# Kernel tuning notes

Hardware: AMD Instinct MI355X
Metric: run time of the kernel (lower is better)

The kernel has to match this reference:

```python
import jax, jax.numpy as jnp
import numpy as np

TAU = 1.5      # lif_tau
V_TH = 1.0     # spikingjelly default v_threshold
EPS = 1e-5     # BatchNorm eps
ALPHA = 4.0    # spikingjelly default sigmoid surrogate alpha

@jax.custom_vjp
def spike_fn(x):
    return (x >= 0.0).astype(x.dtype)

def _spike_fwd(x):
    return spike_fn(x), x

def _spike_bwd(x, g):
    s = jax.nn.sigmoid(ALPHA * x)
    return (g * ALPHA * s * (1.0 - s),)

spike_fn.defvjp(_spike_fwd, _spike_bwd)

def lif(x):
    # x: [T, B, C, N]; hard reset to 0, decay_input=True, detach_reset=True
    def step(v, xt):
        v = v + (xt - v) / TAU
        s = spike_fn(v - V_TH)
        sd = jax.lax.stop_gradient(s)
        v = (1.0 - sd) * v
        return v, s
    _, spikes = jax.lax.scan(step, jnp.zeros_like(x[0]), x)
    return spikes

def bn(x, gamma, beta, mean, var):
    # eval-mode BatchNorm1d over channel dim of [B, C, L]
    inv = gamma * jax.lax.rsqrt(var + EPS)
    return x * inv[None, :, None] + (beta - mean * inv)[None, :, None]

def setup_inputs() -> dict:
    key = jax.random.key(0)
    ks = jax.random.split(key, 13)
    B, C, T, N, H = 8, 256, 4, 4096, 1024
    return {
        "x": jax.random.normal(ks[0], (B, C, T, N), jnp.float32),
        "fc1_w": jax.random.normal(ks[1], (H, C), jnp.float32) * 0.05,
        "fc1_b": jax.random.normal(ks[2], (H,), jnp.float32) * 0.05,
        "fc2_w": jax.random.normal(ks[3], (C, H), jnp.float32) * 0.05,
        "fc2_b": jax.random.normal(ks[4], (C,), jnp.float32) * 0.05,
        "bn1_gamma": jax.random.uniform(ks[5], (H,), jnp.float32, 0.5, 1.5),
        "bn1_beta": jax.random.normal(ks[6], (H,), jnp.float32) * 0.1,
        "bn1_mean": jax.random.normal(ks[7], (H,), jnp.float32) * 0.1,
        "bn1_var": jax.random.uniform(ks[8], (H,), jnp.float32, 0.5, 1.5),
        "bn2_gamma": jax.random.uniform(ks[9], (C,), jnp.float32, 0.5, 1.5),
        "bn2_beta": jax.random.normal(ks[10], (C,), jnp.float32) * 0.1,
        "bn2_mean": jax.random.normal(ks[11], (C,), jnp.float32) * 0.1,
        "bn2_var": jax.random.uniform(ks[12], (C,), jnp.float32, 0.5, 1.5),
    }

def reference(x, fc1_w, fc1_b, fc2_w, fc2_b,
              bn1_gamma, bn1_beta, bn1_mean, bn1_var,
              bn2_gamma, bn2_beta, bn2_mean, bn2_var):
    B, C, T, N = x.shape
    H = fc1_w.shape[0]
    # fc2_bn on raw input, then LIF over T
    h = bn(x.reshape(B, C, T * N), bn2_gamma, bn2_beta, bn2_mean, bn2_var)
    h = h.reshape(B, C, T, N).transpose(2, 0, 1, 3)          # [T,B,C,N]
    h = lif(h).transpose(1, 2, 0, 3).reshape(B, C, T * N)    # [B,C,TN]
    # fc1: 1x1 conv == GEMM over channels
    h = jnp.einsum('hc,bcl->bhl', fc1_w, h) + fc1_b[None, :, None]
    h = bn(h, bn1_gamma, bn1_beta, bn1_mean, bn1_var)
    h = h.reshape(B, H, T, N).transpose(2, 0, 1, 3)          # [T,B,H,N]
    h = lif(h).transpose(1, 2, 0, 3).reshape(B, H, T * N)    # [B,H,TN]
    # fc2
    h = jnp.einsum('ch,bhl->bcl', fc2_w, h) + fc2_b[None, :, None]
    return h.reshape(B, C, T, N)
```

## Files before the change

kernel.cpp:

```cpp
#include <hip/hip_runtime.h>

#define BB 8
#define CC 256
#define TT 4
#define NNv 4096
#define HH 1024
#define LLv (TT*NNv)

typedef short bf16x8 __attribute__((ext_vector_type(8)));
typedef float f32x4 __attribute__((ext_vector_type(4)));

static __device__ __forceinline__ float bfbits2f(unsigned short h) {
    return __uint_as_float(((unsigned int)h) << 16);
}
static __device__ __forceinline__ unsigned short f2bf(float f) {
    unsigned int u = __float_as_uint(f);
    return (unsigned short)((u + 0x7FFFu + ((u >> 16) & 1u)) >> 16);
}
static __device__ __forceinline__ int permpos(int j) { return (j >> 1) + ((j & 1) << 2); }

static __device__ __forceinline__ uint4 spikes8_to_bf16(unsigned long long d) {
    unsigned int lo = (unsigned int)d, hi = (unsigned int)(d >> 32);
    uint4 o;
    o.x = (lo & 0x10001u) * 0x3F80u;
    o.y = (hi & 0x10001u) * 0x3F80u;
    o.z = ((lo >> 8) & 0x10001u) * 0x3F80u;
    o.w = ((hi >> 8) & 0x10001u) * 0x3F80u;
    return o;
}

__global__ __launch_bounds__(256) void k_prep1(const float* __restrict__ w,
                                               unsigned short* __restrict__ wf)
{
    int i = blockIdx.x * 256 + threadIdx.x;
    int h = i >> 8, c = i & 255;
    int ht = h >> 6, hr = h & 63, g = hr >> 4, ln = hr & 15;
    int ko = c >> 6, cr = c & 63, kb = cr >> 5, q = (cr >> 3) & 3, j = c & 7;
    size_t base = (((((size_t)ht * 4 + ko) * 2 + kb) * 4 + g) * 64 + q * 16 + ln) * 8 + permpos(j);
    const size_t WS = 262144;
    float x = w[i];
    unsigned short hi = f2bf(x); float r  = __fsub_rn(x, bfbits2f(hi));
    unsigned short md = f2bf(r); float r2 = __fsub_rn(r, bfbits2f(md));
    unsigned short lo = f2bf(r2);
    wf[base] = hi; wf[WS + base] = md; wf[2 * WS + base] = lo;
}

__global__ __launch_bounds__(256) void k_prep2(const float* __restrict__ w,
                                               unsigned short* __restrict__ wf)
{
    int i = blockIdx.x * 256 + threadIdx.x;
    int c = i >> 10, h = i & 1023;
    int ct = c >> 6, cr = c & 63, g = cr >> 4, ln = cr & 15;
    int ko = h >> 7, hr = h & 127, kb = hr >> 5, q = (hr >> 3) & 3, j = h & 7;
    size_t base = (((((size_t)ct * 8 + ko) * 4 + kb) * 4 + g) * 64 + q * 16 + ln) * 8 + permpos(j);
    const size_t WS = 262144;
    float x = w[i];
    unsigned short hi = f2bf(x); float r = __fsub_rn(x, bfbits2f(hi));
    unsigned short lo = f2bf(r);
    wf[base] = hi; wf[WS + base] = lo;
}

__global__ __launch_bounds__(256) void k_bn2_lif_t(
    const float* __restrict__ x,
    const float* __restrict__ g, const float* __restrict__ be,
    const float* __restrict__ mu, const float* __restrict__ va,
    unsigned char* __restrict__ s1T)
{
    __shared__ unsigned char ts[TT][64][80];
    int tx = threadIdx.x;
    int n0 = blockIdx.x * 64;
    int c0 = blockIdx.y * 64;
    int b  = blockIdx.z;
    int cl = tx >> 2, np = tx & 3;
    int c = c0 + cl;
    float rsq = __fdiv_rn(1.0f, __fsqrt_rn(__fadd_rn(va[c], 1e-5f)));
    float inv = __fmul_rn(g[c], rsq);
    float add = __fsub_rn(be[c], __fmul_rn(mu[c], inv));
    size_t xb = ((size_t)(b * CC + c) * TT) * NNv + n0 + np * 16;
    float v[16];
    #pragma unroll
    for (int i = 0; i < 16; i++) v[i] = 0.0f;
    #pragma unroll
    for (int t = 0; t < TT; t++) {
        float4 p[4];
        #pragma unroll
        for (int k = 0; k < 4; k++) p[k] = *(const float4*)(x + xb + (size_t)t * NNv + 4 * k);
        const float* xp = (const float*)p;
        unsigned int ob[4] = {0, 0, 0, 0};
        #pragma unroll
        for (int i = 0; i < 16; i++) {
            float y = __fadd_rn(__fmul_rn(xp[i], inv), add);
            float vv = __fadd_rn(v[i], __fdiv_rn(__fsub_rn(y, v[i]), 1.5f));
            bool sp = vv >= 1.0f;
            v[i] = sp ? 0.0f : vv;
            if (sp) ob[i >> 2] |= 1u << (8 * (i & 3));
        }
        uint4 pk; pk.x = ob[0]; pk.y = ob[1]; pk.z = ob[2]; pk.w = ob[3];
        *(uint4*)&ts[t][cl][np * 16] = pk;
    }
    __syncthreads();
    int nl = tx >> 2, cp = tx & 3;
    #pragma unroll
    for (int t = 0; t < TT; t++) {
        unsigned int u[4];
        #pragma unroll
        for (int kk = 0; kk < 4; kk++) {
            u[kk] = (unsigned int)ts[t][cp * 16 + kk * 4 + 0][nl]
                  | ((unsigned int)ts[t][cp * 16 + kk * 4 + 1][nl] << 8)
                  | ((unsigned int)ts[t][cp * 16 + kk * 4 + 2][nl] << 16)
                  | ((unsigned int)ts[t][cp * 16 + kk * 4 + 3][nl] << 24);
        }
        uint4 pk; pk.x = u[0]; pk.y = u[1]; pk.z = u[2]; pk.w = u[3];
        *(uint4*)(s1T + ((size_t)(b * TT + t) * NNv + n0 + nl) * CC + c0 + cp * 16) = pk;
    }
}

__global__ __launch_bounds__(256) void k_gemm1_lif(
    const unsigned short* __restrict__ w1f,
    const float* __restrict__ b1,
    const float* __restrict__ g1, const float* __restrict__ be1,
    const float* __restrict__ mu1, const float* __restrict__ va1,
    const unsigned char* __restrict__ s1T, unsigned char* __restrict__ s2T)
{
    __shared__ unsigned short Ss[TT][64][72];
    const int tx = threadIdx.x;
    const int n0 = blockIdx.x * 64;
    const int ht = blockIdx.y;
    const int b  = blockIdx.z;
    const int lane = tx & 63, w = tx >> 6;
    const int q = lane >> 4, ln = lane & 15;
    const int mh = (w & 1) * 32, wn = (w >> 1) * 32;
    const int h0 = ht * 64;
    const size_t WS = 262144;

    f32x4 acc[TT][2][2];
    #pragma unroll
    for (int t = 0; t < TT; t++)
    #pragma unroll
    for (int mi = 0; mi < 2; mi++)
    #pragma unroll
    for (int ni = 0; ni < 2; ni++)
        acc[t][mi][ni] = (f32x4){0.f, 0.f, 0.f, 0.f};

    for (int ko = 0; ko < 4; ko++) {
        __syncthreads();
        #pragma unroll
        for (int i = 0; i < 8; i++) {
            int task = i * 256 + tx;
            int cb = task & 7, nr = (task >> 3) & 63, t = task >> 9;
            unsigned long long d = *(const unsigned long long*)(
                s1T + ((size_t)(b * TT + t) * NNv + n0 + nr) * CC + ko * 64 + cb * 8);
            *(uint4*)&Ss[t][nr][cb * 8] = spikes8_to_bf16(d);
        }
        __syncthreads();
        #pragma unroll
        for (int kb = 0; kb < 2; kb++) {
            bf16x8 wf[2][3];
            #pragma unroll
            for (int mi = 0; mi < 2; mi++) {
                int gg = (mh >> 4) + mi;
                size_t fbase = (((((size_t)ht * 4 + ko) * 2 + kb) * 4 + gg) * 64 + lane) * 8;
                #pragma unroll
                for (int s = 0; s < 3; s++)
                    wf[mi][s] = *(const bf16x8*)(w1f + s * WS + fbase);
            }
            #pragma unroll
            for (int t = 0; t < TT; t++) {
                bf16x8 sf0 = *(const bf16x8*)&Ss[t][wn + ln][kb * 32 + q * 8];
                bf16x8 sf1 = *(const bf16x8*)&Ss[t][wn + 16 + ln][kb * 32 + q * 8];
                #pragma unroll
                for (int s = 0; s < 3; s++) {
                    acc[t][0][0] = __builtin_amdgcn_mfma_f32_16x16x32_bf16(wf[0][s], sf0, acc[t][0][0], 0, 0, 0);
                    acc[t][0][1] = __builtin_amdgcn_mfma_f32_16x16x32_bf16(wf[0][s], sf1, acc[t][0][1], 0, 0, 0);
                    acc[t][1][0] = __builtin_amdgcn_mfma_f32_16x16x32_bf16(wf[1][s], sf0, acc[t][1][0], 0, 0, 0);
                    acc[t][1][1] = __builtin_amdgcn_mfma_f32_16x16x32_bf16(wf[1][s], sf1, acc[t][1][1], 0, 0, 0);
                }
            }
        }
    }

    #pragma unroll
    for (int mi = 0; mi < 2; mi++) {
        float invr[4], addr_[4], biasr[4];
        #pragma unroll
        for (int r = 0; r < 4; r++) {
            int h = h0 + mh + mi * 16 + q * 4 + r;
            float rsq = __fdiv_rn(1.0f, __fsqrt_rn(__fadd_rn(va1[h], 1e-5f)));
            invr[r] = __fmul_rn(g1[h], rsq);
            addr_[r] = __fsub_rn(be1[h], __fmul_rn(mu1[h], invr[r]));
            biasr[r] = b1[h];
        }
        #pragma unroll
        for (int ni = 0; ni < 2; ni++) {
            int l_n = n0 + wn + ni * 16 + ln;
            float v4[4] = {0.f, 0.f, 0.f, 0.f};
            #pragma unroll
            for (int t = 0; t < TT; t++) {
                unsigned int pk = 0;
                #pragma unroll
                for (int r = 0; r < 4; r++) {
                    float h1 = __fadd_rn(acc[t][mi][ni][r], biasr[r]);
                    float y  = __fadd_rn(__fmul_rn(h1, invr[r]), addr_[r]);
                    float vv = __fadd_rn(v4[r], __fdiv_rn(__fsub_rn(y, v4[r]), 1.5f));
                    bool sp = vv >= 1.0f;
                    v4[r] = sp ? 0.0f : vv;
                    if (sp) pk |= (1u << (8 * r));
                }
                *(unsigned int*)(s2T + ((size_t)b * LLv + t * NNv + l_n) * HH
                                 + h0 + mh + mi * 16 + q * 4) = pk;
            }
        }
    }
}

__global__ __launch_bounds__(256) void k_gemm2(
    const unsigned short* __restrict__ w2f,
    const float* __restrict__ b2c,
    const unsigned char* __restrict__ s2T, float* __restrict__ outp)
{
    __shared__ unsigned short Ss[128][136];
    const int tx = threadIdx.x;
    const int l0 = blockIdx.x * 128;
    const int ct = blockIdx.y;
    const int b  = blockIdx.z;
    const int lane = tx & 63, w = tx >> 6;
    const int q = lane >> 4, ln = lane & 15;
    const int mc = (w & 1) * 32, wl = (w >> 1) * 64;
    const size_t WS = 262144;

    f32x4 acc[2][4];
    #pragma unroll
    for (int mi = 0; mi < 2; mi++)
    #pragma unroll
    for (int ni = 0; ni < 4; ni++)
        acc[mi][ni] = (f32x4){0.f, 0.f, 0.f, 0.f};

    for (int ko = 0; ko < 8; ko++) {
        __syncthreads();
        #pragma unroll
        for (int i = 0; i < 8; i++) {
            int task = i * 256 + tx;
            int hb = task & 15, lr = task >> 4;
            unsigned long long d = *(const unsigned long long*)(
                s2T + ((size_t)b * LLv + l0 + lr) * HH + ko * 128 + hb * 8);
            *(uint4*)&Ss[lr][hb * 8] = spikes8_to_bf16(d);
        }
        __syncthreads();
        #pragma unroll
        for (int kb = 0; kb < 4; kb++) {
            bf16x8 wf[2][2];
            #pragma unroll
            for (int mi = 0; mi < 2; mi++) {
                int gg = (mc >> 4) + mi;
                size_t fbase = (((((size_t)ct * 8 + ko) * 4 + kb) * 4 + gg) * 64 + lane) * 8;
                #pragma unroll
                for (int s = 0; s < 2; s++)
                    wf[mi][s] = *(const bf16x8*)(w2f + s * WS + fbase);
            }
            bf16x8 sf[4];
            #pragma unroll
            for (int ni = 0; ni < 4; ni++)
                sf[ni] = *(const bf16x8*)&Ss[wl + ni * 16 + ln][kb * 32 + q * 8];
            #pragma unroll
            for (int s = 0; s < 2; s++)
            #pragma unroll
            for (int mi = 0; mi < 2; mi++)
            #pragma unroll
            for (int ni = 0; ni < 4; ni++)
                acc[mi][ni] = __builtin_amdgcn_mfma_f32_16x16x32_bf16(wf[mi][s], sf[ni], acc[mi][ni], 0, 0, 0);
        }
    }
    #pragma unroll
    for (int mi = 0; mi < 2; mi++)
    #pragma unroll
    for (int r = 0; r < 4; r++) {
        int c = ct * 64 + mc + mi * 16 + q * 4 + r;
        float bias = b2c[c];
        #pragma unroll
        for (int ni = 0; ni < 4; ni++) {
            int l = l0 + wl + ni * 16 + ln;
            outp[((size_t)b * CC + c) * LLv + l] = __fadd_rn(acc[mi][ni][r], bias);
        }
    }
}

extern "C" void kernel_launch(void* const* d_in, const int* in_sizes, int n_in,
                              void* d_out, int out_size, void* d_ws, size_t ws_size,
                              hipStream_t stream) {
    const float* x    = (const float*)d_in[0];
    const float* fc1w = (const float*)d_in[1];
    const float* fc1b = (const float*)d_in[2];
    const float* fc2w = (const float*)d_in[3];
    const float* fc2b = (const float*)d_in[4];
    const float* g1   = (const float*)d_in[5];
    const float* be1  = (const float*)d_in[6];
    const float* mu1  = (const float*)d_in[7];
    const float* va1  = (const float*)d_in[8];
    const float* g2   = (const float*)d_in[9];
    const float* be2  = (const float*)d_in[10];
    const float* mu2  = (const float*)d_in[11];
    const float* va2  = (const float*)d_in[12];

    unsigned short* w1f = (unsigned short*)d_ws;
    unsigned short* w2f = w1f + (size_t)3 * 262144;
    unsigned char*  s1T = (unsigned char*)(w2f + (size_t)2 * 262144);
    unsigned char*  s2T = s1T + (size_t)BB * CC * LLv;
    float* outp = (float*)d_out;

    hipLaunchKernelGGL(k_prep1, dim3(1024), dim3(256), 0, stream, fc1w, w1f);
    hipLaunchKernelGGL(k_prep2, dim3(1024), dim3(256), 0, stream, fc2w, w2f);
    hipLaunchKernelGGL(k_bn2_lif_t, dim3(NNv / 64, CC / 64, BB), dim3(256), 0, stream,
                       x, g2, be2, mu2, va2, s1T);
    hipLaunchKernelGGL(k_gemm1_lif, dim3(NNv / 64, HH / 64, BB), dim3(256), 0, stream,
                       w1f, fc1b, g1, be1, mu1, va1, s1T, s2T);
    hipLaunchKernelGGL(k_gemm2, dim3(LLv / 128, CC / 64, BB), dim3(256), 0, stream,
                       w2f, fc2b, s2T, outp);
}
```

Baseline: 622.2 us.

## Store spikes as pre-permuted bf16 and load MFMA operands directly from global

Spike tensors are now written as bf16 values in the MFMA operand permutation, so the GEMM kernels read B fragments straight from global memory instead of staging and expanding them through LDS with barriers. The GEMMs are launched in chunks of two batches, and the grid is reordered so blocks sharing an activation tile run adjacently. This keeps the per-chunk s2 intermediate small enough to stay in cache. Launch bounds request higher occupancy. The cost is doubled spike storage and more launches.

```diff
diff --git a/kernel.cpp b/kernel.cpp
--- a/kernel.cpp
+++ b/kernel.cpp
@@ -19,16 +19,6 @@
 }
 static __device__ __forceinline__ int permpos(int j) { return (j >> 1) + ((j & 1) << 2); }
 
-static __device__ __forceinline__ uint4 spikes8_to_bf16(unsigned long long d) {
-    unsigned int lo = (unsigned int)d, hi = (unsigned int)(d >> 32);
-    uint4 o;
-    o.x = (lo & 0x10001u) * 0x3F80u;
-    o.y = (hi & 0x10001u) * 0x3F80u;
-    o.z = ((lo >> 8) & 0x10001u) * 0x3F80u;
-    o.w = ((hi >> 8) & 0x10001u) * 0x3F80u;
-    return o;
-}
-
 __global__ __launch_bounds__(256) void k_prep1(const float* __restrict__ w,
                                                unsigned short* __restrict__ wf)
 {
@@ -64,7 +54,7 @@
     const float* __restrict__ x,
     const float* __restrict__ g, const float* __restrict__ be,
     const float* __restrict__ mu, const float* __restrict__ va,
-    unsigned char* __restrict__ s1T)
+    unsigned short* __restrict__ s1b)
 {
     __shared__ unsigned char ts[TT][64][80];
     int tx = threadIdx.x;
@@ -100,33 +90,31 @@
     }
     __syncthreads();
     int nl = tx >> 2, cp = tx & 3;
+    const int perm8[8] = {0, 2, 4, 6, 1, 3, 5, 7};
     #pragma unroll
     for (int t = 0; t < TT; t++) {
-        unsigned int u[4];
-        #pragma unroll
-        for (int kk = 0; kk < 4; kk++) {
-            u[kk] = (unsigned int)ts[t][cp * 16 + kk * 4 + 0][nl]
-                  | ((unsigned int)ts[t][cp * 16 + kk * 4 + 1][nl] << 8)
-                  | ((unsigned int)ts[t][cp * 16 + kk * 4 + 2][nl] << 16)
-                  | ((unsigned int)ts[t][cp * 16 + kk * 4 + 3][nl] << 24);
-        }
-        uint4 pk; pk.x = u[0]; pk.y = u[1]; pk.z = u[2]; pk.w = u[3];
-        *(uint4*)(s1T + ((size_t)(b * TT + t) * NNv + n0 + nl) * CC + c0 + cp * 16) = pk;
-    }
-}
-
-__global__ __launch_bounds__(256) void k_gemm1_lif(
+        unsigned short sh[16];
+        #pragma unroll
+        for (int p = 0; p < 16; p++)
+            sh[p] = ts[t][cp * 16 + (p & 8) + perm8[p & 7]][nl] ? 0x3F80 : 0;
+        unsigned short* op = s1b + ((size_t)(b * TT + t) * NNv + n0 + nl) * CC + c0 + cp * 16;
+        *(uint4*)op = *(uint4*)&sh[0];
+        *(uint4*)(op + 8) = *(uint4*)&sh[8];
+    }
+}
+
+__global__ __launch_bounds__(256, 3) void k_gemm1_lif(
     const unsigned short* __restrict__ w1f,
     const float* __restrict__ b1,
     const float* __restrict__ g1, const float* __restrict__ be1,
     const float* __restrict__ mu1, const float* __restrict__ va1,
-    const unsigned char* __restrict__ s1T, unsigned char* __restrict__ s2T)
-{
-    __shared__ unsigned short Ss[TT][64][72];
+    const unsigned short* __restrict__ s1b, unsigned short* __restrict__ s2b, int boff)
+{
     const int tx = threadIdx.x;
-    const int n0 = blockIdx.x * 64;
-    const int ht = blockIdx.y;
-    const int b  = blockIdx.z;
+    const int ht = blockIdx.x;
+    const int n0 = blockIdx.y * 64;
+    const int bl = blockIdx.z;
+    const int b  = boff + bl;
     const int lane = tx & 63, w = tx >> 6;
     const int q = lane >> 4, ln = lane & 15;
     const int mh = (w & 1) * 32, wn = (w >> 1) * 32;
@@ -142,32 +130,25 @@
     for (int ni = 0; ni < 2; ni++)
         acc[t][mi][ni] = (f32x4){0.f, 0.f, 0.f, 0.f};
 
+    #pragma unroll
     for (int ko = 0; ko < 4; ko++) {
-        __syncthreads();
-        #pragma unroll
-        for (int i = 0; i < 8; i++) {
-            int task = i * 256 + tx;
-            int cb = task & 7, nr = (task >> 3) & 63, t = task >> 9;
-            unsigned long long d = *(const unsigned long long*)(
-                s1T + ((size_t)(b * TT + t) * NNv + n0 + nr) * CC + ko * 64 + cb * 8);
-            *(uint4*)&Ss[t][nr][cb * 8] = spikes8_to_bf16(d);
-        }
-        __syncthreads();
         #pragma unroll
         for (int kb = 0; kb < 2; kb++) {
             bf16x8 wf[2][3];
             #pragma unroll
             for (int mi = 0; mi < 2; mi++) {
                 int gg = (mh >> 4) + mi;
-                size_t fbase = (((((size_t)ht * 4 + ko) * 2 + kb) * 4 + gg) * 64 + lane) * 8;
+                size_t fb = (((((size_t)ht * 4 + ko) * 2 + kb) * 4 + gg) * 64 + lane) * 8;
                 #pragma unroll
                 for (int s = 0; s < 3; s++)
-                    wf[mi][s] = *(const bf16x8*)(w1f + s * WS + fbase);
+                    wf[mi][s] = *(const bf16x8*)(w1f + s * WS + fb);
             }
             #pragma unroll
             for (int t = 0; t < TT; t++) {
-                bf16x8 sf0 = *(const bf16x8*)&Ss[t][wn + ln][kb * 32 + q * 8];
-                bf16x8 sf1 = *(const bf16x8*)&Ss[t][wn + 16 + ln][kb * 32 + q * 8];
+                const unsigned short* bp = s1b
+                    + ((size_t)(b * TT + t) * NNv + n0 + wn) * CC + ko * 64 + kb * 32 + q * 8;
+                bf16x8 sf0 = *(const bf16x8*)(bp + ln * CC);
+                bf16x8 sf1 = *(const bf16x8*)(bp + (16 + ln) * CC);
                 #pragma unroll
                 for (int s = 0; s < 3; s++) {
                     acc[t][0][0] = __builtin_amdgcn_mfma_f32_16x16x32_bf16(wf[0][s], sf0, acc[t][0][0], 0, 0, 0);
@@ -190,13 +171,15 @@
             addr_[r] = __fsub_rn(be1[h], __fmul_rn(mu1[h], invr[r]));
             biasr[r] = b1[h];
         }
+        int hgrp = h0 + mh + mi * 16 + (q >> 1) * 8;
+        int hsub = (q & 1) * 2;
         #pragma unroll
         for (int ni = 0; ni < 2; ni++) {
             int l_n = n0 + wn + ni * 16 + ln;
             float v4[4] = {0.f, 0.f, 0.f, 0.f};
             #pragma unroll
             for (int t = 0; t < TT; t++) {
-                unsigned int pk = 0;
+                unsigned short sv[4];
                 #pragma unroll
                 for (int r = 0; r < 4; r++) {
                     float h1 = __fadd_rn(acc[t][mi][ni][r], biasr[r]);
@@ -204,25 +187,26 @@
                     float vv = __fadd_rn(v4[r], __fdiv_rn(__fsub_rn(y, v4[r]), 1.5f));
                     bool sp = vv >= 1.0f;
                     v4[r] = sp ? 0.0f : vv;
-                    if (sp) pk |= (1u << (8 * r));
+                    sv[r] = sp ? 0x3F80 : 0;
                 }
-                *(unsigned int*)(s2T + ((size_t)b * LLv + t * NNv + l_n) * HH
-                                 + h0 + mh + mi * 16 + q * 4) = pk;
-            }
-        }
-    }
-}
-
-__global__ __launch_bounds__(256) void k_gemm2(
+                unsigned short* op = s2b + ((size_t)bl * LLv + t * NNv + l_n) * HH + hgrp + hsub;
+                *(unsigned int*)op       = (unsigned int)sv[0] | ((unsigned int)sv[2] << 16);
+                *(unsigned int*)(op + 4) = (unsigned int)sv[1] | ((unsigned int)sv[3] << 16);
+            }
+        }
+    }
+}
+
+__global__ __launch_bounds__(256, 4) void k_gemm2(
     const unsigned short* __restrict__ w2f,
     const float* __restrict__ b2c,
-    const unsigned char* __restrict__ s2T, float* __restrict__ outp)
-{
-    __shared__ unsigned short Ss[128][136];
+    const unsigned short* __restrict__ s2b, float* __restrict__ outp, int boff)
+{
     const int tx = threadIdx.x;
-    const int l0 = blockIdx.x * 128;
-    const int ct = blockIdx.y;
-    const int b  = blockIdx.z;
+    const int ct = blockIdx.x;
+    const int l0 = blockIdx.y * 128;
+    const int bl = blockIdx.z;
+    const int b  = boff + bl;
     const int lane = tx & 63, w = tx >> 6;
     const int q = lane >> 4, ln = lane & 15;
     const int mc = (w & 1) * 32, wl = (w >> 1) * 64;
@@ -235,32 +219,25 @@
     for (int ni = 0; ni < 4; ni++)
         acc[mi][ni] = (f32x4){0.f, 0.f, 0.f, 0.f};
 
+    #pragma unroll
     for (int ko = 0; ko < 8; ko++) {
-        __syncthreads();
-        #pragma unroll
-        for (int i = 0; i < 8; i++) {
-            int task = i * 256 + tx;
-            int hb = task & 15, lr = task >> 4;
-            unsigned long long d = *(const unsigned long long*)(
-                s2T + ((size_t)b * LLv + l0 + lr) * HH + ko * 128 + hb * 8);
-            *(uint4*)&Ss[lr][hb * 8] = spikes8_to_bf16(d);
-        }
-        __syncthreads();
         #pragma unroll
         for (int kb = 0; kb < 4; kb++) {
             bf16x8 wf[2][2];
             #pragma unroll
             for (int mi = 0; mi < 2; mi++) {
                 int gg = (mc >> 4) + mi;
-                size_t fbase = (((((size_t)ct * 8 + ko) * 4 + kb) * 4 + gg) * 64 + lane) * 8;
+                size_t fb = (((((size_t)ct * 8 + ko) * 4 + kb) * 4 + gg) * 64 + lane) * 8;
                 #pragma unroll
                 for (int s = 0; s < 2; s++)
-                    wf[mi][s] = *(const bf16x8*)(w2f + s * WS + fbase);
+                    wf[mi][s] = *(const bf16x8*)(w2f + s * WS + fb);
             }
             bf16x8 sf[4];
+            const unsigned short* bp = s2b
+                + ((size_t)bl * LLv + l0 + wl) * HH + ko * 128 + kb * 32 + q * 8;
             #pragma unroll
             for (int ni = 0; ni < 4; ni++)
-                sf[ni] = *(const bf16x8*)&Ss[wl + ni * 16 + ln][kb * 32 + q * 8];
+                sf[ni] = *(const bf16x8*)(bp + (ni * 16 + ln) * HH);
             #pragma unroll
             for (int s = 0; s < 2; s++)
             #pragma unroll
@@ -301,18 +278,21 @@
     const float* mu2  = (const float*)d_in[11];
     const float* va2  = (const float*)d_in[12];
 
+    const size_t WS = 262144;
     unsigned short* w1f = (unsigned short*)d_ws;
-    unsigned short* w2f = w1f + (size_t)3 * 262144;
-    unsigned char*  s1T = (unsigned char*)(w2f + (size_t)2 * 262144);
-    unsigned char*  s2T = s1T + (size_t)BB * CC * LLv;
+    unsigned short* w2f = w1f + 3 * WS;
+    unsigned short* s1b = w2f + 2 * WS;
+    unsigned short* s2b = s1b + (size_t)BB * CC * LLv;
     float* outp = (float*)d_out;
 
     hipLaunchKernelGGL(k_prep1, dim3(1024), dim3(256), 0, stream, fc1w, w1f);
     hipLaunchKernelGGL(k_prep2, dim3(1024), dim3(256), 0, stream, fc2w, w2f);
     hipLaunchKernelGGL(k_bn2_lif_t, dim3(NNv / 64, CC / 64, BB), dim3(256), 0, stream,
-                       x, g2, be2, mu2, va2, s1T);
-    hipLaunchKernelGGL(k_gemm1_lif, dim3(NNv / 64, HH / 64, BB), dim3(256), 0, stream,
-                       w1f, fc1b, g1, be1, mu1, va1, s1T, s2T);
-    hipLaunchKernelGGL(k_gemm2, dim3(LLv / 128, CC / 64, BB), dim3(256), 0, stream,
-                       w2f, fc2b, s2T, outp);
-}
+                       x, g2, be2, mu2, va2, s1b);
+    for (int boff = 0; boff < BB; boff += 2) {
+        hipLaunchKernelGGL(k_gemm1_lif, dim3(HH / 64, NNv / 64, 2), dim3(256), 0, stream,
+                           w1f, fc1b, g1, be1, mu1, va1, s1b, s2b, boff);
+        hipLaunchKernelGGL(k_gemm2, dim3(CC / 64, LLv / 128, 2), dim3(256), 0, stream,
+                           w2f, fc2b, s2b, outp, boff);
+    }
+}
```

After: 1.022 ms. +64.2%, slower.
